# Performance work log

Measured on AMD Instinct MI355X. Metric: run time of the kernel, lower is better.

Reference implementation:

```python
import jax, jax.numpy as jnp
import numpy as np

N_NODES = 100000
N_EDGES = 1600000
D = 128
L = 3


def setup_inputs() -> dict:
    key = jax.random.key(0)
    ks = jax.random.split(key, 5)
    x = jax.random.normal(ks[0], (N_NODES, D), dtype=jnp.float32)
    # Xavier-ish scale for stability through 3 layers
    scale = 1.0 / np.sqrt(D)
    W_self = jax.random.normal(ks[1], (L, D, D), dtype=jnp.float32) * scale
    W_neigh = jax.random.normal(ks[2], (L, D, D), dtype=jnp.float32) * scale
    bias = jnp.zeros((L, D), dtype=jnp.float32)
    src = jax.random.randint(ks[3], (N_EDGES,), 0, N_NODES)
    dst = jax.random.randint(ks[4], (N_EDGES,), 0, N_NODES)
    return {"x": x, "W_self": W_self, "W_neigh": W_neigh, "bias": bias,
            "src": src, "dst": dst}


def reference(x, W_self, W_neigh, bias, src, dst):
    """HomoSAGEEncoder forward (inference mode, dropout = identity).

    Each layer: DGL SAGEConv('mean'):
        h_neigh[v] = mean_{u in in-neighbors(v)} h[u]   (0 if no neighbors)
        h = h @ W_self + h_neigh @ W_neigh + bias
    followed by ReLU.
    """
    N = x.shape[0]
    n_layers = W_self.shape[0]
    # in-degree per destination node (shared across layers)
    deg = jax.ops.segment_sum(jnp.ones_like(dst, dtype=x.dtype), dst,
                              num_segments=N)
    inv_deg = (1.0 / jnp.maximum(deg, 1.0))[:, None]  # [N,1]

    h = x
    for l in range(n_layers):
        msg = h[src]  # [E,D] gather
        h_neigh = jax.ops.segment_sum(msg, dst, num_segments=N) * inv_deg
        h = h @ W_self[l] + h_neigh @ W_neigh[l] + bias[l]
        h = jax.nn.relu(h)
        # dropout is identity at inference; skipped
    return h
```

## Files before the change

kernel.cpp:

```cpp
#include <hip/hip_runtime.h>

typedef __attribute__((ext_vector_type(8))) short short8;
typedef __attribute__((ext_vector_type(4))) float f32x4;

static constexpr int NN = 100000;
static constexpr int NE = 1600000;
static constexpr int DD = 128;
static constexpr int SCAN_CHUNK = 1024;
static constexpr int NB = (NN + SCAN_CHUNK - 1) / SCAN_CHUNK;
static constexpr int NBUCK = 98;
static constexpr int CAP = 18432;

static constexpr int OFF_DEG  = 0;
static constexpr int OFF_OFFS = NN;
static constexpr int OFF_CUR  = 2*NN + 2;
static constexpr int OFF_GCUR = 3*NN + 8;
static constexpr int OFF_PART = 3*NN + 136;
static constexpr int OFF_INV  = 3*NN + 264;
static constexpr int OFF_WT   = 4*NN + 264;
static constexpr int OFF_SS   = 4*NN + 49416;
static constexpr int OFF_HB   = 4*NN + 49416 + NE;
static constexpr int OFF_HNB  = OFF_HB + NN*64;
static constexpr int ZERO_BASE = OFF_CUR;
static constexpr int ZERO_N    = NN + 134;

__device__ inline ushort f2b(float f) {
  uint u = __builtin_bit_cast(uint, f);
  uint r = (u + 0x7fffu + ((u >> 16) & 1u)) >> 16;
  return (ushort)r;
}
__device__ inline float b2f(ushort b) {
  uint u = ((uint)b) << 16;
  return __builtin_bit_cast(float, u);
}

__global__ void k_zero(int* p) {
  int i = blockIdx.x * blockDim.x + threadIdx.x;
  if (i < ZERO_N) p[i] = 0;
}

__global__ void k_x2b(const float* __restrict__ x, ushort* __restrict__ hb) {
  int i = blockIdx.x * blockDim.x + threadIdx.x;
  if (i < NN * (DD / 2)) {
    float2 v = *(const float2*)(x + (size_t)i * 2);
    uint p = (uint)f2b(v.x) | ((uint)f2b(v.y) << 16);
    *(uint*)(hb + (size_t)i * 2) = p;
  }
}

__global__ void k_wt(const float* __restrict__ Ws, const float* __restrict__ Wn,
                     ushort* __restrict__ Wt) {
  int i = blockIdx.x * blockDim.x + threadIdx.x;
  if (i < 3 * 128 * 256) {
    int l = i >> 15;
    int rem = i & 32767;
    int col = rem >> 8;
    int k = rem & 255;
    float v = (k < 128) ? Ws[((size_t)l * 128 + k) * 128 + col]
                        : Wn[((size_t)l * 128 + (k - 128)) * 128 + col];
    Wt[i] = f2b(v);
  }
}

__global__ __launch_bounds__(256) void k_bucket(const int* __restrict__ src,
                                                const int* __restrict__ dst,
                                                int* __restrict__ gcur,
                                                int2* __restrict__ ebuf) {
  __shared__ int cnt[NBUCK], base[NBUCK];
  int t = threadIdx.x;
  int b0 = blockIdx.x * 4096;
  if (t < NBUCK) cnt[t] = 0;
  __syncthreads();
  int dv[16], pv[16];
#pragma unroll
  for (int j = 0; j < 16; ++j) {
    int idx = b0 + j * 256 + t;
    if (idx < NE) {
      int d = dst[idx];
      dv[j] = d;
      pv[j] = atomicAdd(&cnt[d >> 10], 1);
    } else dv[j] = -1;
  }
  __syncthreads();
  if (t < NBUCK) base[t] = atomicAdd(&gcur[t], cnt[t]);
  __syncthreads();
#pragma unroll
  for (int j = 0; j < 16; ++j) {
    if (dv[j] >= 0) {
      int idx = b0 + j * 256 + t;
      int b = dv[j] >> 10;
      int2 pr; pr.x = src[idx]; pr.y = dv[j];
      ebuf[(size_t)b * CAP + base[b] + pv[j]] = pr;
    }
  }
}

__global__ __launch_bounds__(256) void k_hist2(const int2* __restrict__ ebuf,
                                               const int* __restrict__ gcur,
                                               int* __restrict__ deg) {
  __shared__ int hist[1024];
  int b = blockIdx.x, t = threadIdx.x;
#pragma unroll
  for (int j = 0; j < 4; ++j) hist[t + j * 256] = 0;
  __syncthreads();
  int n = gcur[b];
  const int2* eb = ebuf + (size_t)b * CAP;
  for (int i = t; i < n; i += 256) atomicAdd(&hist[eb[i].y & 1023], 1);
  __syncthreads();
#pragma unroll
  for (int j = 0; j < 4; ++j) {
    int node = b * 1024 + t + j * 256;
    if (node < NN) deg[node] = hist[t + j * 256];
  }
}

__global__ void k_scan1(const int* __restrict__ deg, int* __restrict__ offs,
                        int* __restrict__ partials) {
  __shared__ int sc[256];
  int b = blockIdx.x, t = threadIdx.x;
  int base = b * SCAN_CHUNK + t * 4;
  int d0 = (base + 0 < NN) ? deg[base + 0] : 0;
  int d1 = (base + 1 < NN) ? deg[base + 1] : 0;
  int d2 = (base + 2 < NN) ? deg[base + 2] : 0;
  int d3 = (base + 3 < NN) ? deg[base + 3] : 0;
  int s = d0 + d1 + d2 + d3;
  sc[t] = s;
  __syncthreads();
  for (int off = 1; off < 256; off <<= 1) {
    int v = (t >= off) ? sc[t - off] : 0;
    __syncthreads();
    sc[t] += v;
    __syncthreads();
  }
  int ebase = sc[t] - s;
  if (base + 0 < NN) offs[base + 0] = ebase;
  if (base + 1 < NN) offs[base + 1] = ebase + d0;
  if (base + 2 < NN) offs[base + 2] = ebase + d0 + d1;
  if (base + 3 < NN) offs[base + 3] = ebase + d0 + d1 + d2;
  if (t == 255) partials[b] = sc[255];
}

__global__ void k_scan2(int* __restrict__ partials) {
  __shared__ int sc[128];
  int t = threadIdx.x;
  int p = (t < NB) ? partials[t] : 0;
  sc[t] = p;
  __syncthreads();
  for (int off = 1; off < 128; off <<= 1) {
    int v = (t >= off) ? sc[t - off] : 0;
    __syncthreads();
    sc[t] += v;
    __syncthreads();
  }
  if (t < NB) partials[t] = sc[t] - p;
}

__global__ void k_scan3(const int* __restrict__ deg, int* __restrict__ offs,
                        const int* __restrict__ partials, float* __restrict__ inv_deg) {
  int i = blockIdx.x * blockDim.x + threadIdx.x;
  if (i < NN) {
    offs[i] += partials[i / SCAN_CHUNK];
    int d = deg[i];
    inv_deg[i] = 1.0f / (float)(d > 1 ? d : 1);
  }
  if (i == 0) offs[NN] = NE;
}

__global__ __launch_bounds__(256) void k_scatter2(const int2* __restrict__ ebuf,
                                                  const int* __restrict__ gcur,
                                                  const int* __restrict__ offs,
                                                  int* __restrict__ cur,
                                                  int* __restrict__ ss) {
  int b = blockIdx.x >> 2, q = blockIdx.x & 3, t = threadIdx.x;
  int n = gcur[b];
  int lo = (int)((long long)n * q / 4), hi = (int)((long long)n * (q + 1) / 4);
  const int2* eb = ebuf + (size_t)b * CAP;
  for (int i = lo + t; i < hi; i += 256) {
    int2 e = eb[i];
    int pos = offs[e.y] + atomicAdd(&cur[e.y], 1);
    ss[pos] = e.x;
  }
}

__global__ void k_agg2(const ushort* __restrict__ h, const int* __restrict__ offs,
                       const int* __restrict__ ss, const float* __restrict__ inv_deg,
                       ushort* __restrict__ hN) {
  int gid = blockIdx.x * blockDim.x + threadIdx.x;
  int wid = gid >> 6;
  int lane = threadIdx.x & 63;
  int half = lane >> 5, l32 = lane & 31;
  int nw = (gridDim.x * blockDim.x) >> 6;
  for (int vp = wid; vp < NN / 2; vp += nw) {
    int v = vp * 2 + half;
    int beg = offs[v], end = offs[v + 1];
    float a0=0,a1=0,a2=0,a3=0, b0=0,b1=0,b2=0,b3=0;
    float c0=0,c1=0,c2=0,c3=0, d0=0,d1=0,d2=0,d3=0;
    int e = beg;
    for (; e + 3 < end; e += 4) {
      uint2 u0 = *(const uint2*)(h + (size_t)ss[e + 0] * DD + l32 * 4);
      uint2 u1 = *(const uint2*)(h + (size_t)ss[e + 1] * DD + l32 * 4);
      uint2 u2 = *(const uint2*)(h + (size_t)ss[e + 2] * DD + l32 * 4);
      uint2 u3 = *(const uint2*)(h + (size_t)ss[e + 3] * DD + l32 * 4);
      a0 += b2f((ushort)u0.x); a1 += b2f((ushort)(u0.x >> 16));
      a2 += b2f((ushort)u0.y); a3 += b2f((ushort)(u0.y >> 16));
      b0 += b2f((ushort)u1.x); b1 += b2f((ushort)(u1.x >> 16));
      b2 += b2f((ushort)u1.y); b3 += b2f((ushort)(u1.y >> 16));
      c0 += b2f((ushort)u2.x); c1 += b2f((ushort)(u2.x >> 16));
      c2 += b2f((ushort)u2.y); c3 += b2f((ushort)(u2.y >> 16));
      d0 += b2f((ushort)u3.x); d1 += b2f((ushort)(u3.x >> 16));
      d2 += b2f((ushort)u3.y); d3 += b2f((ushort)(u3.y >> 16));
    }
    for (; e < end; ++e) {
      uint2 u0 = *(const uint2*)(h + (size_t)ss[e] * DD + l32 * 4);
      a0 += b2f((ushort)u0.x); a1 += b2f((ushort)(u0.x >> 16));
      a2 += b2f((ushort)u0.y); a3 += b2f((ushort)(u0.y >> 16));
    }
    float w = inv_deg[v];
    float f0 = (a0 + b0) + (c0 + d0);
    float f1 = (a1 + b1) + (c1 + d1);
    float f2 = (a2 + b2) + (c2 + d2);
    float f3 = (a3 + b3) + (c3 + d3);
    f0 *= w; f1 *= w; f2 *= w; f3 *= w;
    uint2 p;
    p.x = (uint)f2b(f0) | ((uint)f2b(f1) << 16);
    p.y = (uint)f2b(f2) | ((uint)f2b(f3) << 16);
    *(uint2*)(hN + (size_t)v * DD + l32 * 4) = p;
  }
}

__global__ __launch_bounds__(256) void k_gemm_mfma(
    const ushort* __restrict__ hA, const ushort* __restrict__ hNb,
    const ushort* __restrict__ Wt, const float* __restrict__ bias,
    ushort* __restrict__ hOutB, float* __restrict__ outF, int writeF) {
  int w = threadIdx.x >> 6;
  int lane = threadIdx.x & 63;
  int row0 = blockIdx.x * 128 + w * 32;
  int r = lane & 15;
  int kg = lane >> 4;

  f32x4 acc[2][8];
#pragma unroll
  for (int mt = 0; mt < 2; ++mt)
#pragma unroll
    for (int nt = 0; nt < 8; ++nt) acc[mt][nt] = (f32x4)0.f;

  int ra0 = row0 + r;       if (ra0 >= NN) ra0 = NN - 1;
  int ra1 = row0 + 16 + r;  if (ra1 >= NN) ra1 = NN - 1;

#pragma unroll
  for (int kt = 0; kt < 8; ++kt) {
    const ushort* hs = (kt < 4) ? hA : hNb;
    int kk = (kt & 3) * 32 + kg * 8;
    short8 a0 = *(const short8*)(hs + (size_t)ra0 * DD + kk);
    short8 a1 = *(const short8*)(hs + (size_t)ra1 * DD + kk);
    int kw = kt * 32 + kg * 8;
#pragma unroll
    for (int nt = 0; nt < 8; ++nt) {
      short8 b = *(const short8*)(Wt + (size_t)(nt * 16 + r) * 256 + kw);
      acc[0][nt] = __builtin_amdgcn_mfma_f32_16x16x32_bf16(a0, b, acc[0][nt], 0, 0, 0);
      acc[1][nt] = __builtin_amdgcn_mfma_f32_16x16x32_bf16(a1, b, acc[1][nt], 0, 0, 0);
    }
  }

  float bv[8];
#pragma unroll
  for (int nt = 0; nt < 8; ++nt) bv[nt] = bias[nt * 16 + r];

  int kg4 = kg * 4;
#pragma unroll
  for (int mt = 0; mt < 2; ++mt) {
#pragma unroll
    for (int j = 0; j < 4; ++j) {
      int row = row0 + mt * 16 + kg4 + j;
      if (row < NN) {
#pragma unroll
        for (int nt = 0; nt < 8; ++nt) {
          float val = fmaxf(acc[mt][nt][j] + bv[nt], 0.f);
          hOutB[(size_t)row * DD + nt * 16 + r] = f2b(val);
          if (writeF) outF[(size_t)row * DD + nt * 16 + r] = val;
        }
      }
    }
  }
}

extern "C" void kernel_launch(void* const* d_in, const int* in_sizes, int n_in,
                              void* d_out, int out_size, void* d_ws, size_t ws_size,
                              hipStream_t stream) {
  const float* x    = (const float*)d_in[0];
  const float* Ws   = (const float*)d_in[1];
  const float* Wn   = (const float*)d_in[2];
  const float* bias = (const float*)d_in[3];
  const int*   src  = (const int*)d_in[4];
  const int*   dst  = (const int*)d_in[5];
  float* out = (float*)d_out;

  int* ws      = (int*)d_ws;
  int* deg     = ws + OFF_DEG;
  int* offs    = ws + OFF_OFFS;
  int* cur     = ws + OFF_CUR;
  int* gcur    = ws + OFF_GCUR;
  int* part    = ws + OFF_PART;
  float* inv   = (float*)(ws + OFF_INV);
  ushort* Wt   = (ushort*)(ws + OFF_WT);
  int* ssorted = ws + OFF_SS;
  ushort* hB   = (ushort*)(ws + OFF_HB);
  ushort* hNb  = (ushort*)(ws + OFF_HNB);
  int2* ebuf   = (int2*)(ws + OFF_HNB);

  k_zero<<<(ZERO_N + 255) / 256, 256, 0, stream>>>(ws + ZERO_BASE);
  k_x2b<<<(NN * (DD / 2) + 255) / 256, 256, 0, stream>>>(x, hB);
  k_wt<<<(3 * 128 * 256 + 255) / 256, 256, 0, stream>>>(Ws, Wn, Wt);
  k_bucket<<<(NE + 4095) / 4096, 256, 0, stream>>>(src, dst, gcur, ebuf);
  k_hist2<<<NBUCK, 256, 0, stream>>>(ebuf, gcur, deg);
  k_scan1<<<NB, 256, 0, stream>>>(deg, offs, part);
  k_scan2<<<1, 128, 0, stream>>>(part);
  k_scan3<<<(NN + 255) / 256, 256, 0, stream>>>(deg, offs, part, inv);
  k_scatter2<<<NBUCK * 4, 256, 0, stream>>>(ebuf, gcur, offs, cur, ssorted);

  for (int l = 0; l < 3; ++l) {
    k_agg2<<<2048, 256, 0, stream>>>(hB, offs, ssorted, inv, hNb);
    k_gemm_mfma<<<(NN + 127) / 128, 256, 0, stream>>>(
        hB, hNb, Wt + (size_t)l * 256 * 128, bias + l * DD, hB, out, l == 2 ? 1 : 0);
  }
}
```

Before: 609.8 us.

## Fuse CSR build into per-bucket LDS sort and widen aggregation loads

The CSR construction is reworked. Buckets become 512 nodes wide (196 buckets), a small scan gives each bucket its base, and one kernel per bucket builds the degree histogram, scans it, writes offsets and inverse degrees, and sorts sources in shared memory before writing them out coalesced. This replaces the hist/scan1/scan2/scan3/scatter2 chain and its global atomics. The aggregation kernel now assigns 16 lanes per node with 16-byte loads and 8-edge unrolling, with one node per quarter-wave and no grid-stride loop. The cost is a large LDS footprint per sort block (about 41KB) and reliance on the bucket capacity bound.

```diff
diff --git a/kernel.cpp b/kernel.cpp
--- a/kernel.cpp
+++ b/kernel.cpp
@@ -6,23 +6,17 @@
 static constexpr int NN = 100000;
 static constexpr int NE = 1600000;
 static constexpr int DD = 128;
-static constexpr int SCAN_CHUNK = 1024;
-static constexpr int NB = (NN + SCAN_CHUNK - 1) / SCAN_CHUNK;
-static constexpr int NBUCK = 98;
-static constexpr int CAP = 18432;
-
-static constexpr int OFF_DEG  = 0;
-static constexpr int OFF_OFFS = NN;
-static constexpr int OFF_CUR  = 2*NN + 2;
-static constexpr int OFF_GCUR = 3*NN + 8;
-static constexpr int OFF_PART = 3*NN + 136;
-static constexpr int OFF_INV  = 3*NN + 264;
-static constexpr int OFF_WT   = 4*NN + 264;
-static constexpr int OFF_SS   = 4*NN + 49416;
-static constexpr int OFF_HB   = 4*NN + 49416 + NE;
-static constexpr int OFF_HNB  = OFF_HB + NN*64;
-static constexpr int ZERO_BASE = OFF_CUR;
-static constexpr int ZERO_N    = NN + 134;
+static constexpr int NBUCK = 196;
+static constexpr int CAP = 9216;
+
+static constexpr int OFF_GCUR  = 0;
+static constexpr int OFF_BBASE = 256;
+static constexpr int OFF_OFFS  = 512;
+static constexpr int OFF_INV   = 100516;
+static constexpr int OFF_WT    = 200520;
+static constexpr int OFF_SS    = 249680;
+static constexpr int OFF_HB    = 1849680;
+static constexpr int OFF_HNB   = 8249680;
 
 __device__ inline ushort f2b(float f) {
   uint u = __builtin_bit_cast(uint, f);
@@ -36,7 +30,7 @@
 
 __global__ void k_zero(int* p) {
   int i = blockIdx.x * blockDim.x + threadIdx.x;
-  if (i < ZERO_N) p[i] = 0;
+  if (i < 256) p[i] = 0;
 }
 
 __global__ void k_x2b(const float* __restrict__ x, ushort* __restrict__ hb) {
@@ -78,7 +72,7 @@
     if (idx < NE) {
       int d = dst[idx];
       dv[j] = d;
-      pv[j] = atomicAdd(&cnt[d >> 10], 1);
+      pv[j] = atomicAdd(&cnt[d >> 9], 1);
     } else dv[j] = -1;
   }
   __syncthreads();
@@ -88,144 +82,123 @@
   for (int j = 0; j < 16; ++j) {
     if (dv[j] >= 0) {
       int idx = b0 + j * 256 + t;
-      int b = dv[j] >> 10;
+      int b = dv[j] >> 9;
       int2 pr; pr.x = src[idx]; pr.y = dv[j];
       ebuf[(size_t)b * CAP + base[b] + pv[j]] = pr;
     }
   }
 }
 
-__global__ __launch_bounds__(256) void k_hist2(const int2* __restrict__ ebuf,
-                                               const int* __restrict__ gcur,
-                                               int* __restrict__ deg) {
-  __shared__ int hist[1024];
+__global__ void k_bscan(const int* __restrict__ gcur, int* __restrict__ bbase) {
+  __shared__ int sc[256];
+  int t = threadIdx.x;
+  int v = (t < NBUCK) ? gcur[t] : 0;
+  sc[t] = v;
+  __syncthreads();
+  for (int off = 1; off < 256; off <<= 1) {
+    int u = (t >= off) ? sc[t - off] : 0;
+    __syncthreads();
+    sc[t] += u;
+    __syncthreads();
+  }
+  if (t < NBUCK) bbase[t] = sc[t] - v;
+  if (t == 255) bbase[NBUCK] = sc[255];
+}
+
+__global__ __launch_bounds__(256) void k_sort(const int2* __restrict__ ebuf,
+                                              const int* __restrict__ bbase,
+                                              int* __restrict__ offs,
+                                              float* __restrict__ inv,
+                                              int* __restrict__ ss) {
+  __shared__ int cnt[512];
+  __shared__ int sbase[512];
+  __shared__ int scan[256];
+  __shared__ int sarr[CAP];
   int b = blockIdx.x, t = threadIdx.x;
-#pragma unroll
-  for (int j = 0; j < 4; ++j) hist[t + j * 256] = 0;
-  __syncthreads();
-  int n = gcur[b];
+  int base0 = bbase[b];
+  int n = bbase[b + 1] - base0;
+  cnt[t] = 0; cnt[t + 256] = 0;
+  __syncthreads();
   const int2* eb = ebuf + (size_t)b * CAP;
-  for (int i = t; i < n; i += 256) atomicAdd(&hist[eb[i].y & 1023], 1);
-  __syncthreads();
-#pragma unroll
-  for (int j = 0; j < 4; ++j) {
-    int node = b * 1024 + t + j * 256;
-    if (node < NN) deg[node] = hist[t + j * 256];
-  }
-}
-
-__global__ void k_scan1(const int* __restrict__ deg, int* __restrict__ offs,
-                        int* __restrict__ partials) {
-  __shared__ int sc[256];
-  int b = blockIdx.x, t = threadIdx.x;
-  int base = b * SCAN_CHUNK + t * 4;
-  int d0 = (base + 0 < NN) ? deg[base + 0] : 0;
-  int d1 = (base + 1 < NN) ? deg[base + 1] : 0;
-  int d2 = (base + 2 < NN) ? deg[base + 2] : 0;
-  int d3 = (base + 3 < NN) ? deg[base + 3] : 0;
-  int s = d0 + d1 + d2 + d3;
-  sc[t] = s;
+  for (int i = t; i < n; i += 256) atomicAdd(&cnt[eb[i].y & 511], 1);
+  __syncthreads();
+  int c0 = cnt[2 * t], c1 = cnt[2 * t + 1];
+  int s = c0 + c1;
+  scan[t] = s;
   __syncthreads();
   for (int off = 1; off < 256; off <<= 1) {
-    int v = (t >= off) ? sc[t - off] : 0;
-    __syncthreads();
-    sc[t] += v;
-    __syncthreads();
-  }
-  int ebase = sc[t] - s;
-  if (base + 0 < NN) offs[base + 0] = ebase;
-  if (base + 1 < NN) offs[base + 1] = ebase + d0;
-  if (base + 2 < NN) offs[base + 2] = ebase + d0 + d1;
-  if (base + 3 < NN) offs[base + 3] = ebase + d0 + d1 + d2;
-  if (t == 255) partials[b] = sc[255];
-}
-
-__global__ void k_scan2(int* __restrict__ partials) {
-  __shared__ int sc[128];
-  int t = threadIdx.x;
-  int p = (t < NB) ? partials[t] : 0;
-  sc[t] = p;
-  __syncthreads();
-  for (int off = 1; off < 128; off <<= 1) {
-    int v = (t >= off) ? sc[t - off] : 0;
-    __syncthreads();
-    sc[t] += v;
-    __syncthreads();
-  }
-  if (t < NB) partials[t] = sc[t] - p;
-}
-
-__global__ void k_scan3(const int* __restrict__ deg, int* __restrict__ offs,
-                        const int* __restrict__ partials, float* __restrict__ inv_deg) {
-  int i = blockIdx.x * blockDim.x + threadIdx.x;
-  if (i < NN) {
-    offs[i] += partials[i / SCAN_CHUNK];
-    int d = deg[i];
-    inv_deg[i] = 1.0f / (float)(d > 1 ? d : 1);
-  }
-  if (i == 0) offs[NN] = NE;
-}
-
-__global__ __launch_bounds__(256) void k_scatter2(const int2* __restrict__ ebuf,
-                                                  const int* __restrict__ gcur,
-                                                  const int* __restrict__ offs,
-                                                  int* __restrict__ cur,
-                                                  int* __restrict__ ss) {
-  int b = blockIdx.x >> 2, q = blockIdx.x & 3, t = threadIdx.x;
-  int n = gcur[b];
-  int lo = (int)((long long)n * q / 4), hi = (int)((long long)n * (q + 1) / 4);
-  const int2* eb = ebuf + (size_t)b * CAP;
-  for (int i = lo + t; i < hi; i += 256) {
+    int u = (t >= off) ? scan[t - off] : 0;
+    __syncthreads();
+    scan[t] += u;
+    __syncthreads();
+  }
+  int eb2 = scan[t] - s;
+  sbase[2 * t] = eb2;
+  sbase[2 * t + 1] = eb2 + c0;
+  int g0 = b * 512 + 2 * t, g1 = g0 + 1;
+  if (g0 < NN) {
+    offs[g0] = base0 + eb2;
+    inv[g0] = 1.0f / (float)(c0 > 1 ? c0 : 1);
+  }
+  if (g1 < NN) {
+    offs[g1] = base0 + eb2 + c0;
+    inv[g1] = 1.0f / (float)(c1 > 1 ? c1 : 1);
+  }
+  if (b == NBUCK - 1 && t == 0) offs[NN] = NE;
+  cnt[2 * t] = 0; cnt[2 * t + 1] = 0;
+  __syncthreads();
+  for (int i = t; i < n; i += 256) {
     int2 e = eb[i];
-    int pos = offs[e.y] + atomicAdd(&cur[e.y], 1);
-    ss[pos] = e.x;
-  }
-}
-
-__global__ void k_agg2(const ushort* __restrict__ h, const int* __restrict__ offs,
-                       const int* __restrict__ ss, const float* __restrict__ inv_deg,
-                       ushort* __restrict__ hN) {
+    int ln = e.y & 511;
+    int p = sbase[ln] + atomicAdd(&cnt[ln], 1);
+    sarr[p] = e.x;
+  }
+  __syncthreads();
+  for (int i = t; i < n; i += 256) ss[base0 + i] = sarr[i];
+}
+
+__global__ __launch_bounds__(256) void k_agg3(const ushort* __restrict__ h,
+                                              const int* __restrict__ offs,
+                                              const int* __restrict__ ss,
+                                              const float* __restrict__ inv_deg,
+                                              ushort* __restrict__ hN) {
   int gid = blockIdx.x * blockDim.x + threadIdx.x;
   int wid = gid >> 6;
   int lane = threadIdx.x & 63;
-  int half = lane >> 5, l32 = lane & 31;
-  int nw = (gridDim.x * blockDim.x) >> 6;
-  for (int vp = wid; vp < NN / 2; vp += nw) {
-    int v = vp * 2 + half;
-    int beg = offs[v], end = offs[v + 1];
-    float a0=0,a1=0,a2=0,a3=0, b0=0,b1=0,b2=0,b3=0;
-    float c0=0,c1=0,c2=0,c3=0, d0=0,d1=0,d2=0,d3=0;
-    int e = beg;
-    for (; e + 3 < end; e += 4) {
-      uint2 u0 = *(const uint2*)(h + (size_t)ss[e + 0] * DD + l32 * 4);
-      uint2 u1 = *(const uint2*)(h + (size_t)ss[e + 1] * DD + l32 * 4);
-      uint2 u2 = *(const uint2*)(h + (size_t)ss[e + 2] * DD + l32 * 4);
-      uint2 u3 = *(const uint2*)(h + (size_t)ss[e + 3] * DD + l32 * 4);
-      a0 += b2f((ushort)u0.x); a1 += b2f((ushort)(u0.x >> 16));
-      a2 += b2f((ushort)u0.y); a3 += b2f((ushort)(u0.y >> 16));
-      b0 += b2f((ushort)u1.x); b1 += b2f((ushort)(u1.x >> 16));
-      b2 += b2f((ushort)u1.y); b3 += b2f((ushort)(u1.y >> 16));
-      c0 += b2f((ushort)u2.x); c1 += b2f((ushort)(u2.x >> 16));
-      c2 += b2f((ushort)u2.y); c3 += b2f((ushort)(u2.y >> 16));
-      d0 += b2f((ushort)u3.x); d1 += b2f((ushort)(u3.x >> 16));
-      d2 += b2f((ushort)u3.y); d3 += b2f((ushort)(u3.y >> 16));
-    }
-    for (; e < end; ++e) {
-      uint2 u0 = *(const uint2*)(h + (size_t)ss[e] * DD + l32 * 4);
-      a0 += b2f((ushort)u0.x); a1 += b2f((ushort)(u0.x >> 16));
-      a2 += b2f((ushort)u0.y); a3 += b2f((ushort)(u0.y >> 16));
-    }
-    float w = inv_deg[v];
-    float f0 = (a0 + b0) + (c0 + d0);
-    float f1 = (a1 + b1) + (c1 + d1);
-    float f2 = (a2 + b2) + (c2 + d2);
-    float f3 = (a3 + b3) + (c3 + d3);
-    f0 *= w; f1 *= w; f2 *= w; f3 *= w;
-    uint2 p;
-    p.x = (uint)f2b(f0) | ((uint)f2b(f1) << 16);
-    p.y = (uint)f2b(f2) | ((uint)f2b(f3) << 16);
-    *(uint2*)(hN + (size_t)v * DD + l32 * 4) = p;
-  }
+  int q = lane >> 4, l16 = lane & 15;
+  int v = wid * 4 + q;
+  int beg = offs[v], end = offs[v + 1];
+  float a0 = 0, a1 = 0, a2 = 0, a3 = 0, a4 = 0, a5 = 0, a6 = 0, a7 = 0;
+  const ushort* hp = h + (size_t)l16 * 8;
+#define ACC8(u) { a0 += b2f((ushort)u.x); a1 += b2f((ushort)(u.x >> 16)); \
+                  a2 += b2f((ushort)u.y); a3 += b2f((ushort)(u.y >> 16)); \
+                  a4 += b2f((ushort)u.z); a5 += b2f((ushort)(u.z >> 16)); \
+                  a6 += b2f((ushort)u.w); a7 += b2f((ushort)(u.w >> 16)); }
+  int e = beg;
+  for (; e + 7 < end; e += 8) {
+    uint4 u0 = *(const uint4*)(hp + (size_t)ss[e + 0] * DD);
+    uint4 u1 = *(const uint4*)(hp + (size_t)ss[e + 1] * DD);
+    uint4 u2 = *(const uint4*)(hp + (size_t)ss[e + 2] * DD);
+    uint4 u3 = *(const uint4*)(hp + (size_t)ss[e + 3] * DD);
+    uint4 u4 = *(const uint4*)(hp + (size_t)ss[e + 4] * DD);
+    uint4 u5 = *(const uint4*)(hp + (size_t)ss[e + 5] * DD);
+    uint4 u6 = *(const uint4*)(hp + (size_t)ss[e + 6] * DD);
+    uint4 u7 = *(const uint4*)(hp + (size_t)ss[e + 7] * DD);
+    ACC8(u0) ACC8(u1) ACC8(u2) ACC8(u3) ACC8(u4) ACC8(u5) ACC8(u6) ACC8(u7)
+  }
+  for (; e < end; ++e) {
+    uint4 u0 = *(const uint4*)(hp + (size_t)ss[e] * DD);
+    ACC8(u0)
+  }
+#undef ACC8
+  float w = inv_deg[v];
+  a0 *= w; a1 *= w; a2 *= w; a3 *= w; a4 *= w; a5 *= w; a6 *= w; a7 *= w;
+  uint4 p;
+  p.x = (uint)f2b(a0) | ((uint)f2b(a1) << 16);
+  p.y = (uint)f2b(a2) | ((uint)f2b(a3) << 16);
+  p.z = (uint)f2b(a4) | ((uint)f2b(a5) << 16);
+  p.w = (uint)f2b(a6) | ((uint)f2b(a7) << 16);
+  *(uint4*)(hN + (size_t)v * DD + l16 * 8) = p;
 }
 
 __global__ __launch_bounds__(256) void k_gemm_mfma(
@@ -296,11 +269,9 @@
   float* out = (float*)d_out;
 
   int* ws      = (int*)d_ws;
-  int* deg     = ws + OFF_DEG;
+  int* gcur    = ws + OFF_GCUR;
+  int* bbase   = ws + OFF_BBASE;
   int* offs    = ws + OFF_OFFS;
-  int* cur     = ws + OFF_CUR;
-  int* gcur    = ws + OFF_GCUR;
-  int* part    = ws + OFF_PART;
   float* inv   = (float*)(ws + OFF_INV);
   ushort* Wt   = (ushort*)(ws + OFF_WT);
   int* ssorted = ws + OFF_SS;
@@ -308,18 +279,15 @@
   ushort* hNb  = (ushort*)(ws + OFF_HNB);
   int2* ebuf   = (int2*)(ws + OFF_HNB);
 
-  k_zero<<<(ZERO_N + 255) / 256, 256, 0, stream>>>(ws + ZERO_BASE);
+  k_zero<<<1, 256, 0, stream>>>(gcur);
   k_x2b<<<(NN * (DD / 2) + 255) / 256, 256, 0, stream>>>(x, hB);
   k_wt<<<(3 * 128 * 256 + 255) / 256, 256, 0, stream>>>(Ws, Wn, Wt);
   k_bucket<<<(NE + 4095) / 4096, 256, 0, stream>>>(src, dst, gcur, ebuf);
-  k_hist2<<<NBUCK, 256, 0, stream>>>(ebuf, gcur, deg);
-  k_scan1<<<NB, 256, 0, stream>>>(deg, offs, part);
-  k_scan2<<<1, 128, 0, stream>>>(part);
-  k_scan3<<<(NN + 255) / 256, 256, 0, stream>>>(deg, offs, part, inv);
-  k_scatter2<<<NBUCK * 4, 256, 0, stream>>>(ebuf, gcur, offs, cur, ssorted);
+  k_bscan<<<1, 256, 0, stream>>>(gcur, bbase);
+  k_sort<<<NBUCK, 256, 0, stream>>>(ebuf, bbase, offs, inv, ssorted);
 
   for (int l = 0; l < 3; ++l) {
-    k_agg2<<<2048, 256, 0, stream>>>(hB, offs, ssorted, inv, hNb);
+    k_agg3<<<NN / 4 / 4, 256, 0, stream>>>(hB, offs, ssorted, inv, hNb);
     k_gemm_mfma<<<(NN + 127) / 128, 256, 0, stream>>>(
         hB, hNb, Wt + (size_t)l * 256 * 128, bias + l * DD, hB, out, l == 2 ? 1 : 0);
   }
```

Result: faster. 553.5 us (-9.2%).
